# Kernel optimization log

Measured on AMD Instinct MI355X. Metric: run time of the kernel, lower is better.

Reference implementation:

```python
import jax, jax.numpy as jnp
import numpy as np

N_NODES = 100000


def _deg_inv_sqrt(dst, num_nodes):
    # degree with self-loops (PyG GCNConv default: add_self_loops=True)
    deg = jax.ops.segment_sum(jnp.ones(dst.shape[0], jnp.float32), dst,
                              num_segments=num_nodes) + 1.0
    return jax.lax.rsqrt(deg)


def gcn_conv(x, W, b, src, dst, dis, num_nodes):
    # PyG GCNConv: h = X W; out = D^-1/2 (A + I) D^-1/2 h + b
    h = x @ W                                  # [N, F_out]
    norm = dis[src] * dis[dst]                 # [E]
    msg = h[src] * norm[:, None]               # [E, F_out] (gather)
    out = jax.ops.segment_sum(msg, dst, num_segments=num_nodes)  # scatter-add
    out = out + h * (dis * dis)[:, None]       # self-loop contribution
    return out + b


def setup_inputs() -> dict:
    key = jax.random.key(0)
    ks = jax.random.split(key, 6)
    n, e = N_NODES, 1600000
    in_f, hid_f, out_f = 64, 64, 32
    x = jax.random.normal(ks[0], (n, in_f), jnp.float32)
    edge_index = jax.random.randint(ks[1], (2, e), 0, n, jnp.int64)
    s1 = 1.0 / np.sqrt(in_f)
    s2 = 1.0 / np.sqrt(hid_f)
    W1 = jax.random.normal(ks[2], (in_f, hid_f), jnp.float32) * s1
    b1 = jnp.zeros((hid_f,), jnp.float32)
    W2 = jax.random.normal(ks[3], (hid_f, out_f), jnp.float32) * s2
    b2 = jnp.zeros((out_f,), jnp.float32)
    return {"x": x, "edge_index": edge_index, "W1": W1, "b1": b1,
            "W2": W2, "b2": b2}


def reference(x, edge_index, W1, b1, W2, b2):
    src, dst = edge_index[0], edge_index[1]
    dis = _deg_inv_sqrt(dst, N_NODES)
    h = gcn_conv(x, W1, b1, src, dst, dis, N_NODES)
    h = jax.nn.relu(h)
    return gcn_conv(h, W2, b2, src, dst, dis, N_NODES)
```

## Files before the change

kernel.cpp:

```cpp
#include <hip/hip_runtime.h>
#include <hip/hip_bf16.h>


constexpr int N = 100000;
constexpr int E = 1600000;
constexpr int NBINS = 782;
constexpr int CAP  = 2688;
constexpr int P1B  = 391;
constexpr int GB   = 1563;

__global__ void __launch_bounds__(256) fused_pass1_gemm1(
    const float* __restrict__ x, const float* __restrict__ W1,
    float* __restrict__ h1f,
    const int* __restrict__ src, const int* __restrict__ dst,
    int* __restrict__ cursor, unsigned* __restrict__ rec) {
    __shared__ float ws[64][64];
    __shared__ float xsT[64][64];
    const int bid = blockIdx.x;
    const int t = threadIdx.x;
    if (bid < P1B) {
        int* hist  = (int*)ws;
        int* rbase = hist + 784;
        int* rcur  = rbase + 784;
        for (int i = t; i < 784; i += 256) hist[i] = 0;
        __syncthreads();
        int myd[16], mys[16];
        const int e0 = bid * 4096;
#pragma unroll
        for (int it = 0; it < 16; ++it) {
            int idx = e0 + it * 256 + t;
            bool ok = idx < E;
            myd[it] = ok ? dst[idx] : -1;
            mys[it] = ok ? src[idx] : 0;
            if (ok) atomicAdd(&hist[myd[it] >> 7], 1);
        }
        __syncthreads();
        for (int i = t; i < 784; i += 256) {
            int h = hist[i];
            rbase[i] = (h > 0) ? atomicAdd(&cursor[i], h) : 0;
            rcur[i] = 0;
        }
        __syncthreads();
#pragma unroll
        for (int it = 0; it < 16; ++it) {
            if (myd[it] >= 0) {
                int cb = myd[it] >> 7;
                int r = atomicAdd(&rcur[cb], 1);
                int pos = rbase[cb] + r;
                if (pos < CAP)
                    rec[(size_t)cb * CAP + pos] =
                        ((unsigned)mys[it] << 7) | ((unsigned)myd[it] & 127u);
            }
        }
    } else {
        const int row0 = (bid - P1B) * 64;
        for (int i = t * 4; i < 64 * 64; i += 1024) {
            float4 v = *(const float4*)(W1 + i);
            ws[i >> 6][i & 63]       = v.x;
            ws[i >> 6][(i & 63) + 1] = v.y;
            ws[i >> 6][(i & 63) + 2] = v.z;
            ws[i >> 6][(i & 63) + 3] = v.w;
        }
        {
            const int r  = t & 63;
            const int k0 = (t >> 6) * 16;
            const int gr = row0 + r;
            if (gr < N) {
#pragma unroll
                for (int kk = 0; kk < 16; kk += 4) {
                    float4 v = *(const float4*)(x + (size_t)gr * 64 + k0 + kk);
                    xsT[k0 + kk][r]     = v.x;
                    xsT[k0 + kk + 1][r] = v.y;
                    xsT[k0 + kk + 2][r] = v.z;
                    xsT[k0 + kk + 3][r] = v.w;
                }
            } else {
#pragma unroll
                for (int kk = 0; kk < 16; ++kk) xsT[k0 + kk][r] = 0.0f;
            }
        }
        __syncthreads();
        const int c4 = (t & 15) * 4;
        const int r4 = (t >> 4) * 4;
        float acc[4][4];
#pragma unroll
        for (int i = 0; i < 4; ++i)
#pragma unroll
            for (int j = 0; j < 4; ++j) acc[i][j] = 0.0f;
#pragma unroll 4
        for (int k = 0; k < 64; ++k) {
            float4 wv = *(const float4*)&ws[k][c4];
            float4 xv = *(const float4*)&xsT[k][r4];
            float xa[4] = {xv.x, xv.y, xv.z, xv.w};
            float wa[4] = {wv.x, wv.y, wv.z, wv.w};
#pragma unroll
            for (int i = 0; i < 4; ++i)
#pragma unroll
                for (int j = 0; j < 4; ++j) acc[i][j] += xa[i] * wa[j];
        }
#pragma unroll
        for (int i = 0; i < 4; ++i) {
            const int gr = row0 + r4 + i;
            if (gr < N) {
                *(float4*)(h1f + (size_t)gr * 64 + c4) =
                    make_float4(acc[i][0], acc[i][1], acc[i][2], acc[i][3]);
            }
        }
    }
}

__global__ void __launch_bounds__(256) pass2_kernel(
    const unsigned* __restrict__ rec, const int* __restrict__ cursor,
    const float* __restrict__ h1f, unsigned* __restrict__ pedge,
    int* __restrict__ cnt, __hip_bfloat16* __restrict__ h1p) {
    __shared__ int cur[128];
    __shared__ float dis_s[128];
    const int cb = blockIdx.x;
    const int t = threadIdx.x;
    if (t < 128) cur[t] = 0;
    __syncthreads();
    int m = cursor[cb];
    if (m > CAP) m = CAP;
    const int row0 = cb * 128;
    for (int i = t; i < m; i += 256) {
        unsigned u = rec[(size_t)cb * CAP + i];
        int dl = (int)(u & 127u);
        unsigned s = u >> 7;
        int r = atomicAdd(&cur[dl], 1);
        if (r < 64) pedge[((size_t)(row0 + dl) << 6) + r] = s;
    }
    __syncthreads();
    if (t < 128) {
        const int c = cur[t];
        cnt[row0 + t] = c;
        dis_s[t] = rsqrtf((float)c + 1.0f);
    }
    __syncthreads();
    for (int i = t; i < 2048; i += 256) {
        const int r = i >> 4;
        const int grow = row0 + r;
        if (grow >= N) break;
        const float d = dis_s[r];
        const int c4 = (i & 15) * 4;
        float4 v = *(const float4*)(h1f + (size_t)grow * 64 + c4);
        unsigned short o[4];
        o[0] = __bfloat16_as_ushort(__float2bfloat16(v.x * d));
        o[1] = __bfloat16_as_ushort(__float2bfloat16(v.y * d));
        o[2] = __bfloat16_as_ushort(__float2bfloat16(v.z * d));
        o[3] = __bfloat16_as_ushort(__float2bfloat16(v.w * d));
        *(ushort4*)((unsigned short*)h1p + (size_t)grow * 64 + c4) =
            *(const ushort4*)o;
    }
}

__device__ __forceinline__ void bf8_acc(float* acc, uint4 r) {
    const unsigned u[4] = {r.x, r.y, r.z, r.w};
#pragma unroll
    for (int k = 0; k < 4; ++k) {
        acc[2 * k]     += __uint_as_float(u[k] << 16);
        acc[2 * k + 1] += __uint_as_float(u[k] & 0xffff0000u);
    }
}

__global__ void __launch_bounds__(256) agg1_gemm2_kernel(
    const __hip_bfloat16* __restrict__ h, const unsigned* __restrict__ pedge,
    const int* __restrict__ cnt, const float* __restrict__ b,
    const float* __restrict__ W2, __hip_bfloat16* __restrict__ H2) {
    __shared__ float ws[64][32];
    __shared__ float xs[32][64];
    __shared__ float dis_l[32];
    const int t = threadIdx.x;
    for (int i = t; i < 64 * 32; i += 256) ws[i >> 5][i & 31] = W2[i];

    const int n = blockIdx.x * 32 + (t >> 3);
    const int fq = (t & 7) * 8;
    const unsigned short* hp = (const unsigned short*)h;
    const int c = cnt[n];
    const int deg = (c < 64) ? c : 64;
    const size_t base = (size_t)n << 6;
    float acc[8];
#pragma unroll
    for (int i = 0; i < 8; ++i) acc[i] = 0.0f;
    int j = 0;
    for (; j + 4 <= deg; j += 4) {
        uint4 ss = *(const uint4*)(pedge + base + j);
        uint4 r0 = *(const uint4*)(hp + (size_t)ss.x * 64 + fq);
        uint4 r1 = *(const uint4*)(hp + (size_t)ss.y * 64 + fq);
        uint4 r2 = *(const uint4*)(hp + (size_t)ss.z * 64 + fq);
        uint4 r3 = *(const uint4*)(hp + (size_t)ss.w * 64 + fq);
        bf8_acc(acc, r0);
        bf8_acc(acc, r1);
        bf8_acc(acc, r2);
        bf8_acc(acc, r3);
    }
    if (j + 2 <= deg) {
        uint2 ss = *(const uint2*)(pedge + base + j);
        uint4 r0 = *(const uint4*)(hp + (size_t)ss.x * 64 + fq);
        uint4 r1 = *(const uint4*)(hp + (size_t)ss.y * 64 + fq);
        bf8_acc(acc, r0);
        bf8_acc(acc, r1);
        j += 2;
    }
    if (j < deg) {
        unsigned s0 = pedge[base + j];
        uint4 r0 = *(const uint4*)(hp + (size_t)s0 * 64 + fq);
        bf8_acc(acc, r0);
    }
    uint4 sr = *(const uint4*)(hp + base + fq);
    bf8_acc(acc, sr);
    const float dn = rsqrtf((float)c + 1.0f);
    if ((t & 7) == 0) dis_l[t >> 3] = dn;
    float4 b0 = *(const float4*)(b + fq);
    float4 b1 = *(const float4*)(b + fq + 4);
    float bb[8] = {b0.x, b0.y, b0.z, b0.w, b1.x, b1.y, b1.z, b1.w};
    float* zr = &xs[t >> 3][fq];
#pragma unroll
    for (int i = 0; i < 8; ++i) zr[i] = fmaxf(dn * acc[i] + bb[i], 0.0f);
    __syncthreads();

    const int cc = t & 31;
    const int rb = (t >> 5) * 4;
    float oacc[4] = {0.f, 0.f, 0.f, 0.f};
    for (int k0 = 0; k0 < 64; k0 += 4) {
        float w0 = ws[k0][cc], w1 = ws[k0 + 1][cc];
        float w2 = ws[k0 + 2][cc], w3 = ws[k0 + 3][cc];
#pragma unroll
        for (int i = 0; i < 4; ++i) {
            float4 xv = *(const float4*)&xs[rb + i][k0];
            oacc[i] += xv.x * w0;
            oacc[i] += xv.y * w1;
            oacc[i] += xv.z * w2;
            oacc[i] += xv.w * w3;
        }
    }
#pragma unroll
    for (int i = 0; i < 4; ++i) {
        const int row = blockIdx.x * 32 + rb + i;
        H2[(size_t)row * 32 + cc] = __float2bfloat16(oacc[i] * dis_l[rb + i]);
    }
}

__global__ void __launch_bounds__(256) agg2_kernel(
    const __hip_bfloat16* __restrict__ h, const unsigned* __restrict__ pedge,
    const int* __restrict__ cnt, const float* __restrict__ b,
    float* __restrict__ out) {
    const int wid = (blockIdx.x * blockDim.x + threadIdx.x) >> 6;
    const int lane = threadIdx.x & 63;
    const int n = wid * 16 + (lane >> 2);
    if (n >= N) return;
    const int fq = (lane & 3) * 8;
    const unsigned short* hp = (const unsigned short*)h;
    const int c = cnt[n];
    const int deg = (c < 64) ? c : 64;
    const size_t base = (size_t)n << 6;
    float acc[8];
#pragma unroll
    for (int i = 0; i < 8; ++i) acc[i] = 0.0f;
    int j = 0;
    for (; j + 4 <= deg; j += 4) {
        uint4 ss = *(const uint4*)(pedge + base + j);
        uint4 r0 = *(const uint4*)(hp + (size_t)ss.x * 32 + fq);
        uint4 r1 = *(const uint4*)(hp + (size_t)ss.y * 32 + fq);
        uint4 r2 = *(const uint4*)(hp + (size_t)ss.z * 32 + fq);
        uint4 r3 = *(const uint4*)(hp + (size_t)ss.w * 32 + fq);
        bf8_acc(acc, r0);
        bf8_acc(acc, r1);
        bf8_acc(acc, r2);
        bf8_acc(acc, r3);
    }
    if (j + 2 <= deg) {
        uint2 ss = *(const uint2*)(pedge + base + j);
        uint4 r0 = *(const uint4*)(hp + (size_t)ss.x * 32 + fq);
        uint4 r1 = *(const uint4*)(hp + (size_t)ss.y * 32 + fq);
        bf8_acc(acc, r0);
        bf8_acc(acc, r1);
        j += 2;
    }
    if (j < deg) {
        unsigned s0 = pedge[base + j];
        uint4 r0 = *(const uint4*)(hp + (size_t)s0 * 32 + fq);
        bf8_acc(acc, r0);
    }
    uint4 sr = *(const uint4*)(hp + (size_t)n * 32 + fq);
    bf8_acc(acc, sr);
    const float dn = rsqrtf((float)c + 1.0f);
    float4 b0 = *(const float4*)(b + fq);
    float4 b1 = *(const float4*)(b + fq + 4);
    *(float4*)(out + (size_t)n * 32 + fq) =
        make_float4(dn * acc[0] + b0.x, dn * acc[1] + b0.y,
                    dn * acc[2] + b0.z, dn * acc[3] + b0.w);
    *(float4*)(out + (size_t)n * 32 + fq + 4) =
        make_float4(dn * acc[4] + b1.x, dn * acc[5] + b1.y,
                    dn * acc[6] + b1.z, dn * acc[7] + b1.w);
}

extern "C" void kernel_launch(void* const* d_in, const int* in_sizes, int n_in,
                              void* d_out, int out_size, void* d_ws, size_t ws_size,
                              hipStream_t stream) {
    const float* x  = (const float*)d_in[0];
    const int*   ei = (const int*)d_in[1];
    const float* W1 = (const float*)d_in[2];
    const float* b1 = (const float*)d_in[3];
    const float* W2 = (const float*)d_in[4];
    const float* b2 = (const float*)d_in[5];
    float* out = (float*)d_out;

    const int* src = ei;
    const int* dst = ei + E;

    constexpr size_t NP = 100352;
    int*      cursor = (int*)d_ws;
    int*      cnt    = cursor + 1024;
    unsigned* pedge  = (unsigned*)(cnt + NP);
    unsigned* rec    = pedge + (size_t)N * 64;
    float*    h1f    = (float*)(rec + (size_t)NBINS * CAP);
    __hip_bfloat16* h1p = (__hip_bfloat16*)(h1f + (size_t)N * 64);
    __hip_bfloat16* h2s = h1p + (size_t)N * 64;

    hipMemsetAsync(cursor, 0, 1024 * sizeof(int), stream);
    fused_pass1_gemm1<<<P1B + GB, 256, 0, stream>>>(x, W1, h1f, src, dst,
                                                    cursor, rec);
    pass2_kernel<<<NBINS, 256, 0, stream>>>(rec, cursor, h1f, pedge, cnt, h1p);
    agg1_gemm2_kernel<<<N / 32, 256, 0, stream>>>(h1p, pedge, cnt, b1, W2, h2s);
    agg2_kernel<<<1563, 256, 0, stream>>>(h2s, pedge, cnt, b2, out);
}
```

Baseline: 194.4 us.

## Store GEMM1 output as bf16 and apply source normalization per edge in aggregation

GEMM1 now writes unscaled bf16 features directly instead of fp32. This removes the fp32 write plus the read-back and rescale pass that pass2 used to do. Pass2 now only builds the adjacency and writes a per-node dis array. The layer-1 aggregation gathers dis[src] per edge and scales each neighbour row with an FMA, trading a small extra scattered 4-byte load per edge for less bulk memory traffic. Rounding now happens before the scaling rather than after, which slightly changes numerics.

Result: no change. 191.0 us (-1.8%).

```diff
diff --git a/kernel.cpp b/kernel.cpp
--- a/kernel.cpp
+++ b/kernel.cpp
@@ -11,7 +11,7 @@
 
 __global__ void __launch_bounds__(256) fused_pass1_gemm1(
     const float* __restrict__ x, const float* __restrict__ W1,
-    float* __restrict__ h1f,
+    __hip_bfloat16* __restrict__ h1u,
     const int* __restrict__ src, const int* __restrict__ dst,
     int* __restrict__ cursor, unsigned* __restrict__ rec) {
     __shared__ float ws[64][64];
@@ -102,8 +102,12 @@
         for (int i = 0; i < 4; ++i) {
             const int gr = row0 + r4 + i;
             if (gr < N) {
-                *(float4*)(h1f + (size_t)gr * 64 + c4) =
-                    make_float4(acc[i][0], acc[i][1], acc[i][2], acc[i][3]);
+                unsigned short o[4];
+#pragma unroll
+                for (int j = 0; j < 4; ++j)
+                    o[j] = __bfloat16_as_ushort(__float2bfloat16(acc[i][j]));
+                *(ushort4*)((unsigned short*)h1u + (size_t)gr * 64 + c4) =
+                    *(const ushort4*)o;
             }
         }
     }
@@ -111,10 +115,9 @@
 
 __global__ void __launch_bounds__(256) pass2_kernel(
     const unsigned* __restrict__ rec, const int* __restrict__ cursor,
-    const float* __restrict__ h1f, unsigned* __restrict__ pedge,
-    int* __restrict__ cnt, __hip_bfloat16* __restrict__ h1p) {
+    unsigned* __restrict__ pedge, int* __restrict__ cnt,
+    float* __restrict__ dis) {
     __shared__ int cur[128];
-    __shared__ float dis_s[128];
     const int cb = blockIdx.x;
     const int t = threadIdx.x;
     if (t < 128) cur[t] = 0;
@@ -133,23 +136,7 @@
     if (t < 128) {
         const int c = cur[t];
         cnt[row0 + t] = c;
-        dis_s[t] = rsqrtf((float)c + 1.0f);
-    }
-    __syncthreads();
-    for (int i = t; i < 2048; i += 256) {
-        const int r = i >> 4;
-        const int grow = row0 + r;
-        if (grow >= N) break;
-        const float d = dis_s[r];
-        const int c4 = (i & 15) * 4;
-        float4 v = *(const float4*)(h1f + (size_t)grow * 64 + c4);
-        unsigned short o[4];
-        o[0] = __bfloat16_as_ushort(__float2bfloat16(v.x * d));
-        o[1] = __bfloat16_as_ushort(__float2bfloat16(v.y * d));
-        o[2] = __bfloat16_as_ushort(__float2bfloat16(v.z * d));
-        o[3] = __bfloat16_as_ushort(__float2bfloat16(v.w * d));
-        *(ushort4*)((unsigned short*)h1p + (size_t)grow * 64 + c4) =
-            *(const ushort4*)o;
+        dis[row0 + t] = rsqrtf((float)c + 1.0f);
     }
 }
 
@@ -162,10 +149,20 @@
     }
 }
 
+__device__ __forceinline__ void bf8_fma(float* acc, uint4 r, float w) {
+    const unsigned u[4] = {r.x, r.y, r.z, r.w};
+#pragma unroll
+    for (int k = 0; k < 4; ++k) {
+        acc[2 * k]     += __uint_as_float(u[k] << 16) * w;
+        acc[2 * k + 1] += __uint_as_float(u[k] & 0xffff0000u) * w;
+    }
+}
+
 __global__ void __launch_bounds__(256) agg1_gemm2_kernel(
     const __hip_bfloat16* __restrict__ h, const unsigned* __restrict__ pedge,
-    const int* __restrict__ cnt, const float* __restrict__ b,
-    const float* __restrict__ W2, __hip_bfloat16* __restrict__ H2) {
+    const int* __restrict__ cnt, const float* __restrict__ dis,
+    const float* __restrict__ b, const float* __restrict__ W2,
+    __hip_bfloat16* __restrict__ H2) {
     __shared__ float ws[64][32];
     __shared__ float xs[32][64];
     __shared__ float dis_l[32];
@@ -184,31 +181,34 @@
     int j = 0;
     for (; j + 4 <= deg; j += 4) {
         uint4 ss = *(const uint4*)(pedge + base + j);
+        float w0 = dis[ss.x], w1 = dis[ss.y], w2 = dis[ss.z], w3 = dis[ss.w];
         uint4 r0 = *(const uint4*)(hp + (size_t)ss.x * 64 + fq);
         uint4 r1 = *(const uint4*)(hp + (size_t)ss.y * 64 + fq);
         uint4 r2 = *(const uint4*)(hp + (size_t)ss.z * 64 + fq);
         uint4 r3 = *(const uint4*)(hp + (size_t)ss.w * 64 + fq);
-        bf8_acc(acc, r0);
-        bf8_acc(acc, r1);
-        bf8_acc(acc, r2);
-        bf8_acc(acc, r3);
+        bf8_fma(acc, r0, w0);
+        bf8_fma(acc, r1, w1);
+        bf8_fma(acc, r2, w2);
+        bf8_fma(acc, r3, w3);
     }
     if (j + 2 <= deg) {
         uint2 ss = *(const uint2*)(pedge + base + j);
+        float w0 = dis[ss.x], w1 = dis[ss.y];
         uint4 r0 = *(const uint4*)(hp + (size_t)ss.x * 64 + fq);
         uint4 r1 = *(const uint4*)(hp + (size_t)ss.y * 64 + fq);
-        bf8_acc(acc, r0);
-        bf8_acc(acc, r1);
+        bf8_fma(acc, r0, w0);
+        bf8_fma(acc, r1, w1);
         j += 2;
     }
     if (j < deg) {
         unsigned s0 = pedge[base + j];
+        float w0 = dis[s0];
         uint4 r0 = *(const uint4*)(hp + (size_t)s0 * 64 + fq);
-        bf8_acc(acc, r0);
-    }
+        bf8_fma(acc, r0, w0);
+    }
+    const float dn = dis[n];
     uint4 sr = *(const uint4*)(hp + base + fq);
-    bf8_acc(acc, sr);
-    const float dn = rsqrtf((float)c + 1.0f);
+    bf8_fma(acc, sr, dn);
     if ((t & 7) == 0) dis_l[t >> 3] = dn;
     float4 b0 = *(const float4*)(b + fq);
     float4 b1 = *(const float4*)(b + fq + 4);
@@ -242,8 +242,8 @@
 
 __global__ void __launch_bounds__(256) agg2_kernel(
     const __hip_bfloat16* __restrict__ h, const unsigned* __restrict__ pedge,
-    const int* __restrict__ cnt, const float* __restrict__ b,
-    float* __restrict__ out) {
+    const int* __restrict__ cnt, const float* __restrict__ dis,
+    const float* __restrict__ b, float* __restrict__ out) {
     const int wid = (blockIdx.x * blockDim.x + threadIdx.x) >> 6;
     const int lane = threadIdx.x & 63;
     const int n = wid * 16 + (lane >> 2);
@@ -283,7 +283,7 @@
     }
     uint4 sr = *(const uint4*)(hp + (size_t)n * 32 + fq);
     bf8_acc(acc, sr);
-    const float dn = rsqrtf((float)c + 1.0f);
+    const float dn = dis[n];
     float4 b0 = *(const float4*)(b + fq);
     float4 b1 = *(const float4*)(b + fq + 4);
     *(float4*)(out + (size_t)n * 32 + fq) =
@@ -311,16 +311,17 @@
     constexpr size_t NP = 100352;
     int*      cursor = (int*)d_ws;
     int*      cnt    = cursor + 1024;
-    unsigned* pedge  = (unsigned*)(cnt + NP);
+    float*    dis    = (float*)(cnt + NP);
+    unsigned* pedge  = (unsigned*)(dis + NP);
     unsigned* rec    = pedge + (size_t)N * 64;
-    float*    h1f    = (float*)(rec + (size_t)NBINS * CAP);
-    __hip_bfloat16* h1p = (__hip_bfloat16*)(h1f + (size_t)N * 64);
-    __hip_bfloat16* h2s = h1p + (size_t)N * 64;
+    __hip_bfloat16* h1u = (__hip_bfloat16*)(rec + (size_t)NBINS * CAP);
+    __hip_bfloat16* h2s = h1u + (size_t)N * 64;
 
     hipMemsetAsync(cursor, 0, 1024 * sizeof(int), stream);
-    fused_pass1_gemm1<<<P1B + GB, 256, 0, stream>>>(x, W1, h1f, src, dst,
+    fused_pass1_gemm1<<<P1B + GB, 256, 0, stream>>>(x, W1, h1u, src, dst,
                                                     cursor, rec);
-    pass2_kernel<<<NBINS, 256, 0, stream>>>(rec, cursor, h1f, pedge, cnt, h1p);
-    agg1_gemm2_kernel<<<N / 32, 256, 0, stream>>>(h1p, pedge, cnt, b1, W2, h2s);
-    agg2_kernel<<<1563, 256, 0, stream>>>(h2s, pedge, cnt, b2, out);
-}
+    pass2_kernel<<<NBINS, 256, 0, stream>>>(rec, cursor, pedge, cnt, dis);
+    agg1_gemm2_kernel<<<N / 32, 256, 0, stream>>>(h1u, pedge, cnt, dis, b1, W2,
+                                                  h2s);
+    agg2_kernel<<<1563, 256, 0, stream>>>(h2s, pedge, cnt, dis, b2, out);
+}
```
